# Kernel optimization log

Hardware: AMD Instinct MI355X
Metric: run time of the kernel (lower is better)

The kernel has to match this reference:

```python
import jax, jax.numpy as jnp
import numpy as np

KEEP_PROB = 0.3
KH, KW = 3, 3
STRIDE = (1, 1)
PADDING = ((1, 1), (1, 1))
DILATION = (1, 1)


def setup_inputs() -> dict:
    key = jax.random.key(0)
    k_x, k_w, k_m, k_b = jax.random.split(key, 4)
    B, C_in, H, W = 16, 64, 112, 112
    C_out = 128
    K = C_in * KH * KW  # 576
    x = jax.random.normal(k_x, (B, C_in, H, W), dtype=jnp.float32)
    weight = jax.random.normal(k_w, (C_out, K), dtype=jnp.float32)
    # binary sparsity pattern of the COO tensor, as a float mask
    mask = (jax.random.uniform(k_m, (C_out, K)) < KEEP_PROB).astype(jnp.float32)
    bias = jax.random.normal(k_b, (C_out,), dtype=jnp.float32)
    return {"x": x, "weight": weight, "mask": mask, "bias": bias}


def reference(x, weight, mask, bias):
    # Effective sparse weight matrix [C_out, C_in*kH*kW]
    spW = weight * mask
    # im2col (F.unfold): patches -> [B, C_in*kH*kW, H_out, W_out]
    # ordering of the K axis is (c, i, j) channel-major, matching torch unfold
    patches = jax.lax.conv_general_dilated_patches(
        x,
        filter_shape=(KH, KW),
        window_strides=STRIDE,
        padding=PADDING,
        rhs_dilation=DILATION,
    )  # [B, K, H_out, W_out]
    # sparse.mm(spW, X) + fold(1x1)  ==  GEMM over the K axis
    out = jnp.einsum('ok,bkhw->bohw', spW, patches)
    out = out + bias[None, :, None, None]
    return out
```

## Files before the change

kernel.cpp:

```cpp
#include <hip/hip_runtime.h>
#include <hip/hip_bf16.h>

#define C_IN    64
#define C_OUT   128
#define HH      112
#define WW      112
#define NB      16
#define KTOT    576
#define NSTEPS  36
#define NPIX    (HH*WW)
#define PH      114
#define PPIX    (PH*PH)
#define XT_OFF  147456
#define XT_BYTES ((size_t)NB * PPIX * C_IN * 2)
#define BAND_H  14
#define BH_X    18
#define B_RECS  288
#define A_BYTES 73728
#define B_BYTES 36864
#define TRB     51
#define TY      8
#define TX      16
#define HALO_X  18
#define HALO_P  180
#define TILES_X 7
#define NTILES  98

typedef __bf16 bf16x8 __attribute__((ext_vector_type(8)));
typedef float  f32x16 __attribute__((ext_vector_type(16)));

static __device__ __forceinline__ unsigned short f2bf(float v) {
    unsigned int u = __builtin_bit_cast(unsigned int, v);
    u = u + 0x7fffu + ((u >> 16) & 1u);
    return (unsigned short)(u >> 16);
}

#define GLOAD_LDS(gp, lp) __builtin_amdgcn_global_load_lds( \
    (const __attribute__((address_space(1))) void*)(gp),    \
    (__attribute__((address_space(3))) void*)(lp), 16, 0, 0)

__global__ __launch_bounds__(256) void prep_kernel(
        const float* __restrict__ weight, const float* __restrict__ mask,
        const float* __restrict__ x,
        unsigned short* __restrict__ pw, unsigned short* __restrict__ xT) {
    const int bx  = blockIdx.x;
    const int tid = threadIdx.x;
    if (bx < NSTEPS) {
        const int t  = bx;
        const int mt = tid >> 6;
        const int l  = tid & 63;
        const int g  = l >> 5;
        const int m  = mt * 32 + (l & 31);
        unsigned int words[4];
        #pragma unroll
        for (int ew = 0; ew < 4; ++ew) {
            unsigned int w2[2];
            #pragma unroll
            for (int h = 0; h < 2; ++h) {
                int e    = ew * 2 + h;
                int klog = t * 16 + g * 8 + e;
                int ij   = klog >> 6;
                int c    = klog & 63;
                int ko   = c * 9 + ij;
                w2[h] = f2bf(weight[m * KTOT + ko] * mask[m * KTOT + ko]);
            }
            words[ew] = w2[0] | (w2[1] << 16);
        }
        uint4 o4; o4.x = words[0]; o4.y = words[1]; o4.z = words[2]; o4.w = words[3];
        ((uint4*)pw)[(t * 4 + mt) * 64 + l] = o4;
    } else {
        const int idx = bx - NSTEPS;
        const int b   = idx / TRB;
        const int pp  = (idx % TRB) * 256 + tid;
        if (pp >= PPIX) return;
        const int hp = pp / PH, wp = pp - hp * PH;
        const int gh = hp - 1, gw = wp - 1;
        const bool valid = (unsigned)gh < (unsigned)HH && (unsigned)gw < (unsigned)WW;
        const float* src = x + (size_t)b * C_IN * (HH * WW) + (gh * WW + gw);
        uint4* dst = (uint4*)(xT + ((size_t)b * PPIX + pp) * C_IN);
        #pragma unroll
        for (int cb = 0; cb < 8; ++cb) {
            unsigned int w4[4];
            #pragma unroll
            for (int h = 0; h < 4; ++h) {
                float v0 = valid ? src[(size_t)(cb * 8 + h * 2    ) * (HH * WW)] : 0.0f;
                float v1 = valid ? src[(size_t)(cb * 8 + h * 2 + 1) * (HH * WW)] : 0.0f;
                w4[h] = (unsigned)f2bf(v0) | ((unsigned)f2bf(v1) << 16);
            }
            uint4 o; o.x = w4[0]; o.y = w4[1]; o.z = w4[2]; o.w = w4[3];
            dst[cb] = o;
        }
    }
}

__global__ __launch_bounds__(448, 1) void sparse_conv_band_kernel(
        const unsigned short* __restrict__ xT, const unsigned short* __restrict__ pw,
        const float* __restrict__ bias, float* __restrict__ out) {
    __shared__ __align__(16) unsigned char smem[A_BYTES + 2 * B_BYTES];
    unsigned char* As  = smem;
    unsigned char* Bs0 = smem + A_BYTES;
    unsigned char* Bs1 = smem + A_BYTES + B_BYTES;

    const int bid  = (blockIdx.x & 7) * 32 + (blockIdx.x >> 3);
    const int b    = bid >> 4;
    const int rem  = bid & 15;
    const int mh   = rem & 1;
    const int band = rem >> 1;
    const int h0   = band * BAND_H;
    const int tid  = threadIdx.x;
    const int wave = tid >> 6, l = tid & 63;
    const int g = l >> 5, ln = l & 31;

    const char* xTb = (const char*)xT + (size_t)b * PPIX * (C_IN * 2);

    {
        const char* pwb = (const char*)pw;
        #pragma unroll
        for (int r = 0; r < 10; ++r) {
            int c  = r * 448 + tid;
            int t  = c >> 7;
            int mt = (c >> 6) & 1;
            int ll = c & 63;
            const char* gp = pwb + (size_t)((t * 4 + mh * 2 + mt) * 64 + ll) * 16;
            GLOAD_LDS(gp, (char*)As + r * 7168 + wave * 1024);
        }
        if (tid < 128) {
            int c  = 10 * 448 + tid;
            int t  = c >> 7;
            int mt = (c >> 6) & 1;
            int ll = c & 63;
            const char* gp = pwb + (size_t)((t * 4 + mh * 2 + mt) * 64 + ll) * 16;
            GLOAD_LDS(gp, (char*)As + 10 * 7168 + wave * 1024);
        }
    }

    auto STAGE = [&](int it, unsigned char* dst) {
        const int w0 = it * 16;
        #pragma unroll
        for (int r = 0; r < 5; ++r) {
            int chunk = r * 448 + tid;
            int p = chunk >> 3, s = chunk & 7;
            int yy = p / BH_X, xx = p - yy * BH_X;
            const char* gp = xTb + (size_t)((h0 + yy) * PH + (w0 + xx)) * (C_IN * 2)
                                 + (((s ^ p) & 7) << 4);
            GLOAD_LDS(gp, (char*)dst + r * 7168 + wave * 1024);
        }
        if (tid < 64) {
            int chunk = 5 * 448 + tid;
            int p = chunk >> 3, s = chunk & 7;
            int yy = p / BH_X, xx = p - yy * BH_X;
            const char* gp = xTb + (size_t)((h0 + yy) * PH + (w0 + xx)) * (C_IN * 2)
                                 + (((s ^ p) & 7) << 4);
            GLOAD_LDS(gp, (char*)dst + 5 * 7168 + wave * 1024);
        }
    };

    const int py = 2 * wave + (ln >> 4);
    const int px = ln & 15;

    float bv[2][16];
    #pragma unroll
    for (int mt = 0; mt < 2; ++mt)
        #pragma unroll
        for (int r = 0; r < 16; ++r) {
            int mloc = (r & 3) + 8 * (r >> 2) + 4 * g;
            bv[mt][r] = bias[mh * 64 + mt * 32 + mloc];
        }

    STAGE(0, Bs0);
    __syncthreads();

    const size_t outb = (size_t)b * C_OUT * NPIX;

    #pragma unroll 1
    for (int it = 0; it < 7; ++it) {
        unsigned char* curB = (it & 1) ? Bs1 : Bs0;
        unsigned char* nxtB = (it & 1) ? Bs0 : Bs1;
        if (it < 6) STAGE(it + 1, nxtB);

        f32x16 acc[2];
        #pragma unroll
        for (int mt = 0; mt < 2; ++mt)
            #pragma unroll
            for (int r = 0; r < 16; ++r) acc[mt][r] = bv[mt][r];

        #pragma unroll
        for (int t = 0; t < NSTEPS; ++t) {
            const int ij = t >> 2, cs = t & 3;
            const int di = ij / 3, dj = ij - di * 3;
            const int jb = cs * 2 + g;
            bf16x8 a0 = __builtin_bit_cast(bf16x8,
                *(const uint4*)(As + ((t * 2 + 0) * 64 + l) * 16));
            bf16x8 a1 = __builtin_bit_cast(bf16x8,
                *(const uint4*)(As + ((t * 2 + 1) * 64 + l) * 16));
            const int Pa = (py + di) * BH_X + (px + dj);
            bf16x8 bb = __builtin_bit_cast(bf16x8,
                *(const uint4*)(curB + Pa * 128 + (((jb ^ Pa) & 7) << 4)));
            acc[0] = __builtin_amdgcn_mfma_f32_32x32x16_bf16(a0, bb, acc[0], 0, 0, 0);
            acc[1] = __builtin_amdgcn_mfma_f32_32x32x16_bf16(a1, bb, acc[1], 0, 0, 0);
        }

        #pragma unroll
        for (int mt = 0; mt < 2; ++mt)
            #pragma unroll
            for (int r = 0; r < 16; ++r) {
                int mloc = (r & 3) + 8 * (r >> 2) + 4 * g;
                int o = mh * 64 + mt * 32 + mloc;
                out[outb + (size_t)o * NPIX + (h0 + py) * WW + it * 16 + px] = acc[mt][r];
            }

        if (it < 6) {
            asm volatile("s_waitcnt vmcnt(32)" ::: "memory");
            __builtin_amdgcn_sched_barrier(0);
            __builtin_amdgcn_s_barrier();
        }
    }
}

__global__ __launch_bounds__(256, 4) void sparse_conv_fb_kernel(
        const float* __restrict__ x, const unsigned short* __restrict__ pw,
        const float* __restrict__ bias, float* __restrict__ out) {
    __shared__ __align__(16) unsigned short xs[HALO_P * C_IN];

    const int bid = blockIdx.x;
    const int b   = bid / NTILES;
    const int t98 = bid % NTILES;
    const int tyi = t98 / TILES_X;
    const int txi = t98 % TILES_X;
    const int h0  = tyi * TY, w0 = txi * TX;
    const int tid = threadIdx.x;

    const float* xb = x + (size_t)b * C_IN * HH * WW;
    {
        const int p  = tid;
        const bool act = p < HALO_P;
        int yy = p / HALO_X;
        int xx = p - yy * HALO_X;
        int gh = h0 + yy - 1, gw = w0 + xx - 1;
        const bool valid = act && (unsigned)gh < (unsigned)HH && (unsigned)gw < (unsigned)WW;
        const float* bp = xb + (gh * WW + gw);
        float v[C_IN];
        #pragma unroll
        for (int c = 0; c < C_IN; ++c)
            v[c] = valid ? bp[c * (HH * WW)] : 0.0f;
        if (act) {
            char* xc = (char*)xs + p * (C_IN * 2);
            #pragma unroll
            for (int j = 0; j < 8; ++j) {
                bf16x8 bvv;
                #pragma unroll
                for (int e = 0; e < 8; ++e) bvv[e] = (__bf16)v[j * 8 + e];
                *(uint4*)(xc + (((j ^ p) & 7) << 4)) = __builtin_bit_cast(uint4, bvv);
            }
        }
    }
    __syncthreads();

    const int wave = tid >> 6, l = tid & 63;
    const int wm = wave >> 1, wn = wave & 1;
    const int g  = l >> 5,  ln = l & 31;

    int P0[2];
    #pragma unroll
    for (int ntp = 0; ntp < 2; ++ntp) {
        int pt = wn * 64 + ntp * 32 + ln;
        P0[ntp] = (pt >> 4) * HALO_X + (pt & 15);
    }

    f32x16 acc[2][2];
    #pragma unroll
    for (int i = 0; i < 2; ++i)
        #pragma unroll
        for (int jq = 0; jq < 2; ++jq)
            #pragma unroll
            for (int q = 0; q < 16; ++q) acc[i][jq][q] = 0.0f;

    const uint4* __restrict__ pwv = (const uint4*)pw;

    #pragma unroll 1
    for (int ij = 0; ij < 9; ++ij) {
        const int di = ij / 3;
        const int dj = ij - di * 3;
        const int P0a = P0[0] + di * HALO_X + dj;
        const int P1a = P0[1] + di * HALO_X + dj;
        #pragma unroll
        for (int cs = 0; cs < 4; ++cs) {
            const int t = ij * 4 + cs;
            bf16x8 a0 = __builtin_bit_cast(bf16x8, pwv[(t * 4 + wm * 2 + 0) * 64 + l]);
            bf16x8 a1 = __builtin_bit_cast(bf16x8, pwv[(t * 4 + wm * 2 + 1) * 64 + l]);
            const int jb = cs * 2 + g;
            bf16x8 b0 = __builtin_bit_cast(bf16x8,
                *(const uint4*)((const char*)xs + P0a * (C_IN * 2) + (((jb ^ P0a) & 7) << 4)));
            bf16x8 b1 = __builtin_bit_cast(bf16x8,
                *(const uint4*)((const char*)xs + P1a * (C_IN * 2) + (((jb ^ P1a) & 7) << 4)));
            acc[0][0] = __builtin_amdgcn_mfma_f32_32x32x16_bf16(a0, b0, acc[0][0], 0, 0, 0);
            acc[0][1] = __builtin_amdgcn_mfma_f32_32x32x16_bf16(a0, b1, acc[0][1], 0, 0, 0);
            acc[1][0] = __builtin_amdgcn_mfma_f32_32x32x16_bf16(a1, b0, acc[1][0], 0, 0, 0);
            acc[1][1] = __builtin_amdgcn_mfma_f32_32x32x16_bf16(a1, b1, acc[1][1], 0, 0, 0);
        }
    }

    const size_t outb = (size_t)b * C_OUT * HH * WW;
    #pragma unroll
    for (int mtp = 0; mtp < 2; ++mtp) {
        #pragma unroll
        for (int r = 0; r < 16; ++r) {
            int mloc = (r & 3) + 8 * (r >> 2) + 4 * g;
            int o = (wm * 2 + mtp) * 32 + mloc;
            float bvv = bias[o];
            #pragma unroll
            for (int ntp = 0; ntp < 2; ++ntp) {
                int p  = wn * 64 + ntp * 32 + ln;
                int gh = h0 + (p >> 4), gw = w0 + (p & 15);
                out[outb + ((size_t)o * HH + gh) * WW + gw] = acc[mtp][ntp][r] + bvv;
            }
        }
    }
}

extern "C" void kernel_launch(void* const* d_in, const int* in_sizes, int n_in,
                              void* d_out, int out_size, void* d_ws, size_t ws_size,
                              hipStream_t stream) {
    const float* x    = (const float*)d_in[0];
    const float* w    = (const float*)d_in[1];
    const float* mk   = (const float*)d_in[2];
    const float* bs   = (const float*)d_in[3];
    float* out        = (float*)d_out;
    unsigned short* pw = (unsigned short*)d_ws;

    if (ws_size >= (size_t)XT_OFF + XT_BYTES) {
        unsigned short* xT = (unsigned short*)((char*)d_ws + XT_OFF);
        prep_kernel<<<dim3(NSTEPS + NB * TRB), dim3(256), 0, stream>>>(w, mk, x, pw, xT);
        sparse_conv_band_kernel<<<dim3(256), dim3(448), 0, stream>>>(xT, pw, bs, out);
    } else {
        prep_kernel<<<dim3(NSTEPS), dim3(256), 0, stream>>>(w, mk, x, pw, (unsigned short*)pw);
        sparse_conv_fb_kernel<<<dim3(NB * NTILES), dim3(256), 0, stream>>>(x, pw, bs, out);
    }
}
```

Baseline: 65.38 us.

## Retile band conv to 16-row bands with 4 waves each computing two N-tiles

```diff
diff --git a/kernel.cpp b/kernel.cpp
--- a/kernel.cpp
+++ b/kernel.cpp
@@ -13,11 +13,11 @@
 #define PPIX    (PH*PH)
 #define XT_OFF  147456
 #define XT_BYTES ((size_t)NB * PPIX * C_IN * 2)
-#define BAND_H  14
+#define BAND_H  16
 #define BH_X    18
-#define B_RECS  288
+#define B_RECS  324
 #define A_BYTES 73728
-#define B_BYTES 36864
+#define B_BYTES 41472
 #define TRB     51
 #define TY      8
 #define TX      16
@@ -93,7 +93,7 @@
     }
 }
 
-__global__ __launch_bounds__(448, 1) void sparse_conv_band_kernel(
+__global__ __launch_bounds__(256, 1) void sparse_conv_band_kernel(
         const unsigned short* __restrict__ xT, const unsigned short* __restrict__ pw,
         const float* __restrict__ bias, float* __restrict__ out) {
     __shared__ __align__(16) unsigned char smem[A_BYTES + 2 * B_BYTES];
@@ -101,9 +101,9 @@
     unsigned char* Bs0 = smem + A_BYTES;
     unsigned char* Bs1 = smem + A_BYTES + B_BYTES;
 
-    const int bid  = (blockIdx.x & 7) * 32 + (blockIdx.x >> 3);
-    const int b    = bid >> 4;
-    const int rem  = bid & 15;
+    const int bid  = (blockIdx.x & 7) * 28 + (blockIdx.x >> 3);
+    const int b    = bid / 14;
+    const int rem  = bid % 14;
     const int mh   = rem & 1;
     const int band = rem >> 1;
     const int h0   = band * BAND_H;
@@ -112,51 +112,43 @@
     const int g = l >> 5, ln = l & 31;
 
     const char* xTb = (const char*)xT + (size_t)b * PPIX * (C_IN * 2);
+    const char* pwb = (const char*)pw;
 
     {
-        const char* pwb = (const char*)pw;
-        #pragma unroll
-        for (int r = 0; r < 10; ++r) {
-            int c  = r * 448 + tid;
+        #pragma unroll
+        for (int r = 0; r < 18; ++r) {
+            int c  = r * 256 + tid;
             int t  = c >> 7;
             int mt = (c >> 6) & 1;
             int ll = c & 63;
             const char* gp = pwb + (size_t)((t * 4 + mh * 2 + mt) * 64 + ll) * 16;
-            GLOAD_LDS(gp, (char*)As + r * 7168 + wave * 1024);
-        }
-        if (tid < 128) {
-            int c  = 10 * 448 + tid;
-            int t  = c >> 7;
-            int mt = (c >> 6) & 1;
-            int ll = c & 63;
-            const char* gp = pwb + (size_t)((t * 4 + mh * 2 + mt) * 64 + ll) * 16;
-            GLOAD_LDS(gp, (char*)As + 10 * 7168 + wave * 1024);
+            GLOAD_LDS(gp, (char*)As + r * 4096 + wave * 1024);
         }
     }
 
     auto STAGE = [&](int it, unsigned char* dst) {
         const int w0 = it * 16;
         #pragma unroll
-        for (int r = 0; r < 5; ++r) {
-            int chunk = r * 448 + tid;
+        for (int r = 0; r < 10; ++r) {
+            int chunk = r * 256 + tid;
             int p = chunk >> 3, s = chunk & 7;
             int yy = p / BH_X, xx = p - yy * BH_X;
             const char* gp = xTb + (size_t)((h0 + yy) * PH + (w0 + xx)) * (C_IN * 2)
                                  + (((s ^ p) & 7) << 4);
-            GLOAD_LDS(gp, (char*)dst + r * 7168 + wave * 1024);
-        }
-        if (tid < 64) {
-            int chunk = 5 * 448 + tid;
+            GLOAD_LDS(gp, (char*)dst + r * 4096 + wave * 1024);
+        }
+        if (tid < 32) {
+            int chunk = 10 * 256 + tid;
             int p = chunk >> 3, s = chunk & 7;
             int yy = p / BH_X, xx = p - yy * BH_X;
             const char* gp = xTb + (size_t)((h0 + yy) * PH + (w0 + xx)) * (C_IN * 2)
                                  + (((s ^ p) & 7) << 4);
-            GLOAD_LDS(gp, (char*)dst + 5 * 7168 + wave * 1024);
+            GLOAD_LDS(gp, (char*)dst + 10 * 4096);
         }
     };
 
-    const int py = 2 * wave + (ln >> 4);
     const int px = ln & 15;
+    const int pyb = 4 * wave + (ln >> 4);
 
     float bv[2][16];
     #pragma unroll
@@ -178,11 +170,13 @@
         unsigned char* nxtB = (it & 1) ? Bs0 : Bs1;
         if (it < 6) STAGE(it + 1, nxtB);
 
-        f32x16 acc[2];
+        f32x16 acc[2][2];
         #pragma unroll
         for (int mt = 0; mt < 2; ++mt)
             #pragma unroll
-            for (int r = 0; r < 16; ++r) acc[mt][r] = bv[mt][r];
+            for (int ntp = 0; ntp < 2; ++ntp)
+                #pragma unroll
+                for (int r = 0; r < 16; ++r) acc[mt][ntp][r] = bv[mt][r];
 
         #pragma unroll
         for (int t = 0; t < NSTEPS; ++t) {
@@ -193,11 +187,14 @@
                 *(const uint4*)(As + ((t * 2 + 0) * 64 + l) * 16));
             bf16x8 a1 = __builtin_bit_cast(bf16x8,
                 *(const uint4*)(As + ((t * 2 + 1) * 64 + l) * 16));
-            const int Pa = (py + di) * BH_X + (px + dj);
-            bf16x8 bb = __builtin_bit_cast(bf16x8,
-                *(const uint4*)(curB + Pa * 128 + (((jb ^ Pa) & 7) << 4)));
-            acc[0] = __builtin_amdgcn_mfma_f32_32x32x16_bf16(a0, bb, acc[0], 0, 0, 0);
-            acc[1] = __builtin_amdgcn_mfma_f32_32x32x16_bf16(a1, bb, acc[1], 0, 0, 0);
+            #pragma unroll
+            for (int ntp = 0; ntp < 2; ++ntp) {
+                const int Pa = (pyb + 2 * ntp + di) * BH_X + (px + dj);
+                bf16x8 bb = __builtin_bit_cast(bf16x8,
+                    *(const uint4*)(curB + Pa * 128 + (((jb ^ Pa) & 7) << 4)));
+                acc[0][ntp] = __builtin_amdgcn_mfma_f32_32x32x16_bf16(a0, bb, acc[0][ntp], 0, 0, 0);
+                acc[1][ntp] = __builtin_amdgcn_mfma_f32_32x32x16_bf16(a1, bb, acc[1][ntp], 0, 0, 0);
+            }
         }
 
         #pragma unroll
@@ -206,11 +203,15 @@
             for (int r = 0; r < 16; ++r) {
                 int mloc = (r & 3) + 8 * (r >> 2) + 4 * g;
                 int o = mh * 64 + mt * 32 + mloc;
-                out[outb + (size_t)o * NPIX + (h0 + py) * WW + it * 16 + px] = acc[mt][r];
+                #pragma unroll
+                for (int ntp = 0; ntp < 2; ++ntp) {
+                    int row = h0 + pyb + 2 * ntp;
+                    out[outb + (size_t)o * NPIX + row * WW + it * 16 + px] = acc[mt][ntp][r];
+                }
             }
 
         if (it < 6) {
-            asm volatile("s_waitcnt vmcnt(32)" ::: "memory");
+            asm volatile("s_waitcnt vmcnt(56)" ::: "memory");
             __builtin_amdgcn_sched_barrier(0);
             __builtin_amdgcn_s_barrier();
         }
@@ -331,7 +332,7 @@
     if (ws_size >= (size_t)XT_OFF + XT_BYTES) {
         unsigned short* xT = (unsigned short*)((char*)d_ws + XT_OFF);
         prep_kernel<<<dim3(NSTEPS + NB * TRB), dim3(256), 0, stream>>>(w, mk, x, pw, xT);
-        sparse_conv_band_kernel<<<dim3(256), dim3(448), 0, stream>>>(xT, pw, bs, out);
+        sparse_conv_band_kernel<<<dim3(224), dim3(256), 0, stream>>>(xT, pw, bs, out);
     } else {
         prep_kernel<<<dim3(NSTEPS), dim3(256), 0, stream>>>(w, mk, x, pw, (unsigned short*)pw);
         sparse_conv_fb_kernel<<<dim3(NB * NTILES), dim3(256), 0, stream>>>(x, pw, bs, out);
```

After: 74.30 us. 1.14x slower.

## Widen band tiles to 32 columns with single buffer and 16-column tail

Applied to the files above, without the earlier changes.

```diff
diff --git a/kernel.cpp b/kernel.cpp
--- a/kernel.cpp
+++ b/kernel.cpp
@@ -14,10 +14,12 @@
 #define XT_OFF  147456
 #define XT_BYTES ((size_t)NB * PPIX * C_IN * 2)
 #define BAND_H  14
-#define BH_X    18
-#define B_RECS  288
 #define A_BYTES 73728
-#define B_BYTES 36864
+#define B32_X   34
+#define B32_RECS 544
+#define B16_X   18
+#define B16_RECS 288
+#define B_BYTES 69632
 #define TRB     51
 #define TY      8
 #define TX      16
@@ -96,10 +98,9 @@
 __global__ __launch_bounds__(448, 1) void sparse_conv_band_kernel(
         const unsigned short* __restrict__ xT, const unsigned short* __restrict__ pw,
         const float* __restrict__ bias, float* __restrict__ out) {
-    __shared__ __align__(16) unsigned char smem[A_BYTES + 2 * B_BYTES];
-    unsigned char* As  = smem;
-    unsigned char* Bs0 = smem + A_BYTES;
-    unsigned char* Bs1 = smem + A_BYTES + B_BYTES;
+    __shared__ __align__(16) unsigned char smem[A_BYTES + B_BYTES];
+    unsigned char* As = smem;
+    unsigned char* Bs = smem + A_BYTES;
 
     const int bid  = (blockIdx.x & 7) * 32 + (blockIdx.x >> 3);
     const int b    = bid >> 4;
@@ -112,9 +113,9 @@
     const int g = l >> 5, ln = l & 31;
 
     const char* xTb = (const char*)xT + (size_t)b * PPIX * (C_IN * 2);
+    const char* pwb = (const char*)pw;
 
     {
-        const char* pwb = (const char*)pw;
         #pragma unroll
         for (int r = 0; r < 10; ++r) {
             int c  = r * 448 + tid;
@@ -134,29 +135,45 @@
         }
     }
 
-    auto STAGE = [&](int it, unsigned char* dst) {
-        const int w0 = it * 16;
+    auto STAGE32 = [&](int it) {
+        const int w0 = it * 32;
+        #pragma unroll
+        for (int r = 0; r < 9; ++r) {
+            int chunk = r * 448 + tid;
+            int p = chunk >> 3, s = chunk & 7;
+            int yy = p / B32_X, xx = p - yy * B32_X;
+            const char* gp = xTb + (size_t)((h0 + yy) * PH + (w0 + xx)) * (C_IN * 2)
+                                 + (((s ^ p) & 7) << 4);
+            GLOAD_LDS(gp, (char*)Bs + r * 7168 + wave * 1024);
+        }
+        if (tid < 320) {
+            int chunk = 9 * 448 + tid;
+            int p = chunk >> 3, s = chunk & 7;
+            int yy = p / B32_X, xx = p - yy * B32_X;
+            const char* gp = xTb + (size_t)((h0 + yy) * PH + (w0 + xx)) * (C_IN * 2)
+                                 + (((s ^ p) & 7) << 4);
+            GLOAD_LDS(gp, (char*)Bs + 9 * 7168 + wave * 1024);
+        }
+    };
+    auto STAGE16 = [&]() {
         #pragma unroll
         for (int r = 0; r < 5; ++r) {
             int chunk = r * 448 + tid;
             int p = chunk >> 3, s = chunk & 7;
-            int yy = p / BH_X, xx = p - yy * BH_X;
-            const char* gp = xTb + (size_t)((h0 + yy) * PH + (w0 + xx)) * (C_IN * 2)
+            int yy = p / B16_X, xx = p - yy * B16_X;
+            const char* gp = xTb + (size_t)((h0 + yy) * PH + (96 + xx)) * (C_IN * 2)
                                  + (((s ^ p) & 7) << 4);
-            GLOAD_LDS(gp, (char*)dst + r * 7168 + wave * 1024);
+            GLOAD_LDS(gp, (char*)Bs + r * 7168 + wave * 1024);
         }
         if (tid < 64) {
             int chunk = 5 * 448 + tid;
             int p = chunk >> 3, s = chunk & 7;
-            int yy = p / BH_X, xx = p - yy * BH_X;
-            const char* gp = xTb + (size_t)((h0 + yy) * PH + (w0 + xx)) * (C_IN * 2)
+            int yy = p / B16_X, xx = p - yy * B16_X;
+            const char* gp = xTb + (size_t)((h0 + yy) * PH + (96 + xx)) * (C_IN * 2)
                                  + (((s ^ p) & 7) << 4);
-            GLOAD_LDS(gp, (char*)dst + 5 * 7168 + wave * 1024);
+            GLOAD_LDS(gp, (char*)Bs + 5 * 7168 + wave * 1024);
         }
     };
-
-    const int py = 2 * wave + (ln >> 4);
-    const int px = ln & 15;
 
     float bv[2][16];
     #pragma unroll
@@ -167,22 +184,20 @@
             bv[mt][r] = bias[mh * 64 + mt * 32 + mloc];
         }
 
-    STAGE(0, Bs0);
+    STAGE32(0);
     __syncthreads();
 
     const size_t outb = (size_t)b * C_OUT * NPIX;
 
     #pragma unroll 1
-    for (int it = 0; it < 7; ++it) {
-        unsigned char* curB = (it & 1) ? Bs1 : Bs0;
-        unsigned char* nxtB = (it & 1) ? Bs0 : Bs1;
-        if (it < 6) STAGE(it + 1, nxtB);
-
-        f32x16 acc[2];
+    for (int it = 0; it < 3; ++it) {
+        f32x16 acc[2][2];
         #pragma unroll
         for (int mt = 0; mt < 2; ++mt)
             #pragma unroll
-            for (int r = 0; r < 16; ++r) acc[mt][r] = bv[mt][r];
+            for (int ntp = 0; ntp < 2; ++ntp)
+                #pragma unroll
+                for (int r = 0; r < 16; ++r) acc[mt][ntp][r] = bv[mt][r];
 
         #pragma unroll
         for (int t = 0; t < NSTEPS; ++t) {
@@ -193,12 +208,18 @@
                 *(const uint4*)(As + ((t * 2 + 0) * 64 + l) * 16));
             bf16x8 a1 = __builtin_bit_cast(bf16x8,
                 *(const uint4*)(As + ((t * 2 + 1) * 64 + l) * 16));
-            const int Pa = (py + di) * BH_X + (px + dj);
-            bf16x8 bb = __builtin_bit_cast(bf16x8,
-                *(const uint4*)(curB + Pa * 128 + (((jb ^ Pa) & 7) << 4)));
-            acc[0] = __builtin_amdgcn_mfma_f32_32x32x16_bf16(a0, bb, acc[0], 0, 0, 0);
-            acc[1] = __builtin_amdgcn_mfma_f32_32x32x16_bf16(a1, bb, acc[1], 0, 0, 0);
-        }
+            #pragma unroll
+            for (int ntp = 0; ntp < 2; ++ntp) {
+                const int Pa = (2 * wave + ntp + di) * B32_X + (ln + dj);
+                bf16x8 bb = __builtin_bit_cast(bf16x8,
+                    *(const uint4*)(Bs + Pa * 128 + (((jb ^ Pa) & 7) << 4)));
+                acc[0][ntp] = __builtin_amdgcn_mfma_f32_32x32x16_bf16(a0, bb, acc[0][ntp], 0, 0, 0);
+                acc[1][ntp] = __builtin_amdgcn_mfma_f32_32x32x16_bf16(a1, bb, acc[1][ntp], 0, 0, 0);
+            }
+        }
+
+        __builtin_amdgcn_s_barrier();
+        if (it < 2) STAGE32(it + 1); else STAGE16();
 
         #pragma unroll
         for (int mt = 0; mt < 2; ++mt)
@@ -206,14 +227,51 @@
             for (int r = 0; r < 16; ++r) {
                 int mloc = (r & 3) + 8 * (r >> 2) + 4 * g;
                 int o = mh * 64 + mt * 32 + mloc;
-                out[outb + (size_t)o * NPIX + (h0 + py) * WW + it * 16 + px] = acc[mt][r];
-            }
-
-        if (it < 6) {
-            asm volatile("s_waitcnt vmcnt(32)" ::: "memory");
-            __builtin_amdgcn_sched_barrier(0);
-            __builtin_amdgcn_s_barrier();
-        }
+                #pragma unroll
+                for (int ntp = 0; ntp < 2; ++ntp) {
+                    int row = h0 + 2 * wave + ntp;
+                    out[outb + (size_t)o * NPIX + row * WW + it * 32 + ln] = acc[mt][ntp][r];
+                }
+            }
+
+        asm volatile("s_waitcnt vmcnt(63)" ::: "memory");
+        __builtin_amdgcn_sched_barrier(0);
+        __builtin_amdgcn_s_barrier();
+    }
+
+    {
+        const int px = ln & 15;
+        const int py = 2 * wave + (ln >> 4);
+        f32x16 acc[2];
+        #pragma unroll
+        for (int mt = 0; mt < 2; ++mt)
+            #pragma unroll
+            for (int r = 0; r < 16; ++r) acc[mt][r] = bv[mt][r];
+
+        #pragma unroll
+        for (int t = 0; t < NSTEPS; ++t) {
+            const int ij = t >> 2, cs = t & 3;
+            const int di = ij / 3, dj = ij - di * 3;
+            const int jb = cs * 2 + g;
+            bf16x8 a0 = __builtin_bit_cast(bf16x8,
+                *(const uint4*)(As + ((t * 2 + 0) * 64 + l) * 16));
+            bf16x8 a1 = __builtin_bit_cast(bf16x8,
+                *(const uint4*)(As + ((t * 2 + 1) * 64 + l) * 16));
+            const int Pa = (py + di) * B16_X + (px + dj);
+            bf16x8 bb = __builtin_bit_cast(bf16x8,
+                *(const uint4*)(Bs + Pa * 128 + (((jb ^ Pa) & 7) << 4)));
+            acc[0] = __builtin_amdgcn_mfma_f32_32x32x16_bf16(a0, bb, acc[0], 0, 0, 0);
+            acc[1] = __builtin_amdgcn_mfma_f32_32x32x16_bf16(a1, bb, acc[1], 0, 0, 0);
+        }
+
+        #pragma unroll
+        for (int mt = 0; mt < 2; ++mt)
+            #pragma unroll
+            for (int r = 0; r < 16; ++r) {
+                int mloc = (r & 3) + 8 * (r >> 2) + 4 * g;
+                int o = mh * 64 + mt * 32 + mloc;
+                out[outb + (size_t)o * NPIX + (h0 + py) * WW + 96 + px] = acc[mt][r];
+            }
     }
 }
 
```

Result: slower. 69.80 us (+6.8%).
